# Kernel tuning notes

Hardware: AMD Instinct MI355X
Metric: run time of the kernel (lower is better)

## Reference

```python
import jax, jax.numpy as jnp
import numpy as np

NUM_LATENT, NUM_TRASH, DEPTH = 7, 3, 4
N_QUBITS = NUM_LATENT + NUM_TRASH            # 10, embedding/entangler wires
N_WIRES = NUM_LATENT + 2 * NUM_TRASH + 1     # 14, total device wires (wire 0 = MSB, PennyLane convention)
AUX = N_WIRES - 1                            # swap-test ancilla (last wire)
BATCH = 256

_H = (np.array([[1.0, 1.0], [1.0, -1.0]]) / np.sqrt(2.0)).astype(np.complex64)
_CNOT = np.array([[1, 0, 0, 0], [0, 1, 0, 0], [0, 0, 0, 1], [0, 0, 1, 0]], dtype=np.complex64)
_CSWAP = np.eye(8, dtype=np.complex64)
_CSWAP[[5, 6]] = _CSWAP[[6, 5]]              # swap targets iff control=1: |101> <-> |110>


def _rx(theta):
    # RX(theta) = [[cos(t/2), -i sin(t/2)], [-i sin(t/2), cos(t/2)]]; theta [...] -> [..., 2, 2]
    c = jnp.cos(theta / 2).astype(jnp.complex64)
    s = jnp.sin(theta / 2).astype(jnp.complex64) * (-1j)
    return jnp.stack([jnp.stack([c, s], -1), jnp.stack([s, c], -1)], -2)


def _apply_1q(state, gate, wire):
    # state [B, 2^W]; gate [2,2] (shared) or [B,2,2] (per-sample)
    B = state.shape[0]
    a, b = 2 ** wire, 2 ** (N_WIRES - wire - 1)
    s = state.reshape(B, a, 2, b)
    if gate.ndim == 3:
        s = jnp.einsum('bij,bajc->baic', gate, s)
    else:
        s = jnp.einsum('ij,bajc->baic', gate, s)
    return s.reshape(B, -1)


def _apply_kq(state, gate, wires):
    # general k-qubit constant gate on arbitrary (possibly non-adjacent) wires
    B = state.shape[0]
    k = len(wires)
    t = state.reshape((B,) + (2,) * N_WIRES)
    t = jnp.moveaxis(t, [w + 1 for w in wires], range(1, k + 1))
    t = t.reshape(B, 2 ** k, -1)
    t = jnp.einsum('ij,bjc->bic', jnp.asarray(gate), t)
    t = t.reshape((B,) + (2,) * N_WIRES)
    t = jnp.moveaxis(t, range(1, k + 1), [w + 1 for w in wires])
    return t.reshape(B, -1)


def _forward(features, weights):
    B = features.shape[0]
    state = jnp.zeros((B, 2 ** N_WIRES), jnp.complex64).at[:, 0].set(1.0)
    # AngleEmbedding(rotation='X'): per-sample RX(features[:, w]) on wire w
    g_emb = _rx(features)  # [B, n_qubits, 2, 2]
    for w in range(N_QUBITS):
        state = _apply_1q(state, g_emb[:, w], w)
    # BasicEntanglerLayers: per layer, RX(weights[l, w]) on each wire, then ring of CNOTs
    wts = weights.reshape(DEPTH, N_QUBITS)
    for l in range(DEPTH):
        g_l = _rx(wts[l])  # [n_qubits, 2, 2]
        for w in range(N_QUBITS):
            state = _apply_1q(state, g_l[w], w)
        for w in range(N_QUBITS):
            state = _apply_kq(state, _CNOT, [w, (w + 1) % N_QUBITS])
    # Swap test: H(aux); CSWAP(aux, latent+i, latent+trash+i); H(aux)
    state = _apply_1q(state, jnp.asarray(_H), AUX)
    for i in range(NUM_TRASH):
        state = _apply_kq(state, _CSWAP, [AUX, NUM_LATENT + i, NUM_LATENT + NUM_TRASH + i])
    state = _apply_1q(state, jnp.asarray(_H), AUX)
    # probs on aux wire (last wire -> innermost axis); return P(aux=1)
    p = jnp.sum(jnp.abs(state.reshape(B, 2 ** (N_WIRES - 1), 2)) ** 2, axis=1)
    return p[:, 1]


def setup_inputs() -> dict:
    key = jax.random.key(0)
    kf, kw = jax.random.split(key)
    features = jax.random.normal(kf, (BATCH, N_QUBITS), jnp.float32)
    weights = 0.01 * jax.random.uniform(kw, (DEPTH, N_QUBITS), jnp.float32)
    return {"features": features, "weights": weights}


def reference(features, weights):
    return _forward(features, weights)
```

## Files before the change

### kernel.cpp

```cpp
#include <hip/hip_runtime.h>
#include <math.h>


#define NQ     10
#define DIM    1024
#define NDEPTH 4
#define NGATE  (NQ + NDEPTH * NQ)

__device__ inline int cnot_ring_inv(int i) {
#pragma unroll
    for (int w = NQ - 1; w >= 0; --w) {
        int cb   = (i >> (NQ - 1 - w)) & 1;
        int tpos = NQ - 1 - ((w + 1) % NQ);
        i ^= cb << tpos;
    }
    return i;
}

__global__ __launch_bounds__(512) void qae_kernel(
    const float* __restrict__ features,
    const float* __restrict__ weights,
    float* __restrict__ out)
{
    __shared__ float sre[DIM];
    __shared__ float sim_[DIM];
    __shared__ float gc[NGATE];
    __shared__ float gs[NGATE];
    __shared__ float part[2];

    const int b   = blockIdx.x;
    const int tid = threadIdx.x;

    sre[tid]        = 0.0f;  sim_[tid]        = 0.0f;
    sre[tid + 512]  = 0.0f;  sim_[tid + 512]  = 0.0f;
    if (tid == 0) sre[0] = 1.0f;
    if (tid < NGATE) {
        float ang = (tid < NQ) ? features[b * NQ + tid] : weights[tid - NQ];
        float h = 0.5f * ang;
        gc[tid] = cosf(h);
        gs[tid] = sinf(h);
    }
    __syncthreads();

    auto rx = [&](int w, float c, float s) {
        int bitpos = NQ - 1 - w;
        int mask   = 1 << bitpos;
        int i0 = ((tid >> bitpos) << (bitpos + 1)) | (tid & (mask - 1));
        int i1 = i0 | mask;
        float a0r = sre[i0], a0i = sim_[i0];
        float a1r = sre[i1], a1i = sim_[i1];
        sre[i0]  = fmaf(c, a0r,  s * a1i);
        sim_[i0] = fmaf(c, a0i, -s * a1r);
        sre[i1]  = fmaf(c, a1r,  s * a0i);
        sim_[i1] = fmaf(c, a1i, -s * a0r);
    };

    for (int w = 0; w < NQ; ++w) {
        rx(w, gc[w], gs[w]);
        __syncthreads();
    }

    for (int l = 0; l < NDEPTH; ++l) {
        for (int w = 0; w < NQ; ++w) {
            int g = NQ + l * NQ + w;
            rx(w, gc[g], gs[g]);
            __syncthreads();
        }
        int j0 = tid, j1 = tid + 512;
        int s0 = cnot_ring_inv(j0);
        int s1 = cnot_ring_inv(j1);
        float r0 = sre[s0], m0 = sim_[s0];
        float r1 = sre[s1], m1 = sim_[s1];
        __syncthreads();
        sre[j0] = r0; sim_[j0] = m0;
        sre[j1] = r1; sim_[j1] = m1;
        __syncthreads();
    }

    float acc = 0.0f;
    if (tid < 128) {
        int i = tid << 3;
        acc = sre[i] * sre[i] + sim_[i] * sim_[i];
#pragma unroll
        for (int off = 32; off > 0; off >>= 1)
            acc += __shfl_down(acc, off, 64);
    }
    if (tid == 0)  part[0] = acc;
    if (tid == 64) part[1] = acc;
    __syncthreads();
    if (tid == 0)
        out[b] = 0.5f * (1.0f - (part[0] + part[1]));
}

extern "C" void kernel_launch(void* const* d_in, const int* in_sizes, int n_in,
                              void* d_out, int out_size, void* d_ws, size_t ws_size,
                              hipStream_t stream) {
    const float* features = (const float*)d_in[0];
    const float* weights  = (const float*)d_in[1];
    float*       out      = (float*)d_out;

    int B = in_sizes[0] / NQ;
    qae_kernel<<<B, 512, 0, stream>>>(features, weights, out);
}
```

Measured before the change: 62.54 us.

## Run each sample's state vector in one wavefront's registers with shuffles

```diff
diff --git a/kernel.cpp b/kernel.cpp
--- a/kernel.cpp
+++ b/kernel.cpp
@@ -3,7 +3,6 @@
 
 
 #define NQ     10
-#define DIM    1024
 #define NDEPTH 4
 #define NGATE  (NQ + NDEPTH * NQ)
 
@@ -17,79 +16,97 @@
     return i;
 }
 
-__global__ __launch_bounds__(512) void qae_kernel(
+__device__ inline float readlane_f(float v, int lane) {
+    return __int_as_float(__builtin_amdgcn_readlane(__float_as_int(v), lane));
+}
+
+__global__ __launch_bounds__(64) void qae_kernel(
     const float* __restrict__ features,
     const float* __restrict__ weights,
     float* __restrict__ out)
 {
-    __shared__ float sre[DIM];
-    __shared__ float sim_[DIM];
-    __shared__ float gc[NGATE];
-    __shared__ float gs[NGATE];
-    __shared__ float part[2];
+    __shared__ float2 amp[1024];
 
-    const int b   = blockIdx.x;
-    const int tid = threadIdx.x;
+    const int b    = blockIdx.x;
+    const int lane = threadIdx.x;
 
-    sre[tid]        = 0.0f;  sim_[tid]        = 0.0f;
-    sre[tid + 512]  = 0.0f;  sim_[tid + 512]  = 0.0f;
-    if (tid == 0) sre[0] = 1.0f;
-    if (tid < NGATE) {
-        float ang = (tid < NQ) ? features[b * NQ + tid] : weights[tid - NQ];
+    float cg = 1.0f, sg = 0.0f;
+    if (lane < NGATE) {
+        float ang = (lane < NQ) ? features[b * NQ + lane] : weights[lane - NQ];
         float h = 0.5f * ang;
-        gc[tid] = cosf(h);
-        gs[tid] = sinf(h);
+        cg = cosf(h);
+        sg = sinf(h);
     }
-    __syncthreads();
 
-    auto rx = [&](int w, float c, float s) {
-        int bitpos = NQ - 1 - w;
-        int mask   = 1 << bitpos;
-        int i0 = ((tid >> bitpos) << (bitpos + 1)) | (tid & (mask - 1));
-        int i1 = i0 | mask;
-        float a0r = sre[i0], a0i = sim_[i0];
-        float a1r = sre[i1], a1i = sim_[i1];
-        sre[i0]  = fmaf(c, a0r,  s * a1i);
-        sim_[i0] = fmaf(c, a0i, -s * a1r);
-        sre[i1]  = fmaf(c, a1r,  s * a0i);
-        sim_[i1] = fmaf(c, a1i, -s * a0r);
+    float re[16], im[16];
+#pragma unroll
+    for (int r = 0; r < 16; ++r) { re[r] = 0.0f; im[r] = 0.0f; }
+    if (lane == 0) re[0] = 1.0f;
+
+    const int base_inv = cnot_ring_inv(lane << 4);
+
+    auto rx_lane = [&](int xmask, float c, float s) {
+#pragma unroll
+        for (int r = 0; r < 16; ++r) {
+            float pre = __shfl_xor(re[r], xmask, 64);
+            float pim = __shfl_xor(im[r], xmask, 64);
+            re[r] = fmaf(c, re[r],  s * pim);
+            im[r] = fmaf(c, im[r], -s * pre);
+        }
+    };
+    auto rx_reg = [&](int mask, float c, float s) {
+#pragma unroll
+        for (int r = 0; r < 16; ++r) {
+            if (!(r & mask)) {
+                int r1 = r | mask;
+                float a0r = re[r],  a0i = im[r];
+                float a1r = re[r1], a1i = im[r1];
+                re[r]  = fmaf(c, a0r,  s * a1i);
+                im[r]  = fmaf(c, a0i, -s * a1r);
+                re[r1] = fmaf(c, a1r,  s * a0i);
+                im[r1] = fmaf(c, a1i, -s * a0r);
+            }
+        }
+    };
+    auto rx = [&](int w, int g) {
+        float c = readlane_f(cg, g);
+        float s = readlane_f(sg, g);
+        if (w < 6) rx_lane(1 << (5 - w), c, s);
+        else       rx_reg(1 << (9 - w), c, s);
     };
 
-    for (int w = 0; w < NQ; ++w) {
-        rx(w, gc[w], gs[w]);
-        __syncthreads();
+    auto cnot_ring = [&]() {
+#pragma unroll
+        for (int r = 0; r < 16; ++r) {
+            int i  = (lane << 4) | r;
+            int sl = i ^ (lane & 15);
+            amp[sl] = make_float2(re[r], im[r]);
+        }
+#pragma unroll
+        for (int r = 0; r < 16; ++r) {
+            int src = base_inv ^ cnot_ring_inv(r);
+            int sl  = src ^ ((src >> 4) & 15);
+            float2 v = amp[sl];
+            re[r] = v.x;
+            im[r] = v.y;
+        }
+    };
+
+#pragma unroll
+    for (int w = 0; w < NQ; ++w) rx(w, w);
+
+    for (int l = 0; l < NDEPTH; ++l) {
+#pragma unroll
+        for (int w = 0; w < NQ; ++w) rx(w, NQ + l * NQ + w);
+        cnot_ring();
     }
 
-    for (int l = 0; l < NDEPTH; ++l) {
-        for (int w = 0; w < NQ; ++w) {
-            int g = NQ + l * NQ + w;
-            rx(w, gc[g], gs[g]);
-            __syncthreads();
-        }
-        int j0 = tid, j1 = tid + 512;
-        int s0 = cnot_ring_inv(j0);
-        int s1 = cnot_ring_inv(j1);
-        float r0 = sre[s0], m0 = sim_[s0];
-        float r1 = sre[s1], m1 = sim_[s1];
-        __syncthreads();
-        sre[j0] = r0; sim_[j0] = m0;
-        sre[j1] = r1; sim_[j1] = m1;
-        __syncthreads();
-    }
-
-    float acc = 0.0f;
-    if (tid < 128) {
-        int i = tid << 3;
-        acc = sre[i] * sre[i] + sim_[i] * sim_[i];
+    float acc = re[0]*re[0] + im[0]*im[0] + re[8]*re[8] + im[8]*im[8];
 #pragma unroll
-        for (int off = 32; off > 0; off >>= 1)
-            acc += __shfl_down(acc, off, 64);
-    }
-    if (tid == 0)  part[0] = acc;
-    if (tid == 64) part[1] = acc;
-    __syncthreads();
-    if (tid == 0)
-        out[b] = 0.5f * (1.0f - (part[0] + part[1]));
+    for (int off = 32; off; off >>= 1)
+        acc += __shfl_xor(acc, off, 64);
+    if (lane == 0)
+        out[b] = 0.5f * (1.0f - acc);
 }
 
 extern "C" void kernel_launch(void* const* d_in, const int* in_sizes, int n_in,
@@ -100,5 +117,5 @@
     float*       out      = (float*)d_out;
 
     int B = in_sizes[0] / NQ;
-    qae_kernel<<<B, 512, 0, stream>>>(features, weights, out);
+    qae_kernel<<<B, 64, 0, stream>>>(features, weights, out);
 }
```

New measurement: 64.54 us. +3.2%, slower.
